# Optimization experiments

Hardware: AMD Instinct MI355X
Metric: run time of the kernel (lower is better)

Reference implementation:

```python
import jax, jax.numpy as jnp
import numpy as np

B, D, H, K = 32768, 64, 512, 8
P = 3 * K - 1            # widths(K) + heights(K) + interior derivatives(K-1)
BOUND = 4.0
MIN_BIN = 1e-3           # min bin width/height fraction
MIN_DERIV = 1e-3


def setup_inputs() -> dict:
    key = jax.random.key(0)
    k0, k1, k2, k3 = jax.random.split(key, 4)
    x = jax.random.normal(k0, (B, D), jnp.float32) * 2.0
    W1 = jax.random.normal(k1, (H, D), jnp.float32) / np.sqrt(D)
    b1 = jnp.zeros((H,), jnp.float32)
    W2 = jax.random.normal(k2, (D * P, H), jnp.float32) / np.sqrt(H)
    b2 = jax.random.normal(k3, (D * P,), jnp.float32) * 0.01
    m_in = np.arange(1, D + 1)                      # input degrees 1..D
    m_hid = (np.arange(H) % (D - 1)) + 1            # hidden degrees 1..D-1
    M1 = jnp.asarray((m_hid[:, None] >= m_in[None, :]).astype(np.float32))   # [H, D]
    m_out = (np.arange(D * P) // P) + 1             # output degree = dim index + 1
    M2 = jnp.asarray((m_out[:, None] > m_hid[None, :]).astype(np.float32))   # [D*P, H]
    return {"x": x, "W1": W1, "b1": b1, "W2": W2, "b2": b2, "M1": M1, "M2": M2}


def _rqs(x, w_un, h_un, d_un):
    """Monotonic rational-quadratic spline (elementwise over [B, D]).
    w_un, h_un: [B, D, K] unnormalized widths/heights; d_un: [B, D, K-1].
    Returns (y [B, D], logabsdet [B, D])."""
    f32 = x.dtype
    w = jax.nn.softmax(w_un, axis=-1)
    hh = jax.nn.softmax(h_un, axis=-1)
    w = MIN_BIN + (1.0 - MIN_BIN * K) * w
    hh = MIN_BIN + (1.0 - MIN_BIN * K) * hh
    edge_lo = jnp.full(w.shape[:-1] + (1,), -BOUND, f32)
    edge_hi = jnp.full(w.shape[:-1] + (1,), BOUND, f32)
    # knot positions [B, D, K+1] with exact endpoints at +-BOUND
    xk = jnp.concatenate([edge_lo, -BOUND + 2.0 * BOUND * jnp.cumsum(w, -1)[..., :-1], edge_hi], -1)
    yk = jnp.concatenate([edge_lo, -BOUND + 2.0 * BOUND * jnp.cumsum(hh, -1)[..., :-1], edge_hi], -1)
    widths = xk[..., 1:] - xk[..., :-1]
    heights = yk[..., 1:] - yk[..., :-1]
    ones = jnp.ones(w.shape[:-1] + (1,), f32)
    # boundary derivatives fixed to 1 (identity outside the box)
    d = jnp.concatenate([ones, MIN_DERIV + jax.nn.softplus(d_un), ones], -1)  # [B, D, K+1]

    inside = (x >= -BOUND) & (x <= BOUND)
    xc = jnp.clip(x, -BOUND, BOUND)
    # bucketize: index of containing bin
    idx = jnp.clip(jnp.sum((xc[..., None] >= xk).astype(jnp.int32), -1) - 1, 0, K - 1)

    def g(a, off=0):
        return jnp.take_along_axis(a, idx[..., None] + off, axis=-1)[..., 0]

    x_k, y_k = g(xk), g(yk)
    w_k, h_k = g(widths), g(heights)
    d_k, d_k1 = g(d), g(d, 1)
    s = h_k / w_k
    theta = (xc - x_k) / w_k
    t1m = theta * (1.0 - theta)
    num = h_k * (s * theta * theta + d_k * t1m)
    den = s + (d_k1 + d_k - 2.0 * s) * t1m
    y_in = y_k + num / den
    dnum = s * s * (d_k1 * theta * theta + 2.0 * s * t1m + d_k * (1.0 - theta) ** 2)
    ld_in = jnp.log(dnum) - 2.0 * jnp.log(den)
    y = jnp.where(inside, y_in, x)
    ld = jnp.where(inside, ld_in, 0.0)
    return y, ld


def _forward(x, W1, b1, W2, b2, M1, M2):
    hmid = jax.nn.relu(x @ (W1 * M1).T + b1)          # [B, H]
    params = (hmid @ (W2 * M2).T + b2).reshape(x.shape[0], D, P)
    w_un = params[..., :K]
    h_un = params[..., K:2 * K]
    d_un = params[..., 2 * K:]
    z, ld = _rqs(x, w_un, h_un, d_un)
    return z, jnp.sum(ld, axis=-1)                    # logDet per example


def reference(x, W1, b1, W2, b2, M1, M2):
    return _forward(x, W1, b1, W2, b2, M1, M2)
```

## Files before the change

### kernel.cpp

```cpp
#include <hip/hip_runtime.h>
#include <math.h>

#define NB    32768
#define DDIM  64
#define HDIM  512
#define PDIM  23
#define KBINS 8
#define BM    32
#define NCOLS (DDIM * PDIM)
#define CHUNK 368
#define PSTRIDE 372
#define NTILES 92

#define RQ_BOUND  4.0f
#define RQ_MINBIN 0.001f
#define RQ_MINDER 0.001f

typedef __attribute__((ext_vector_type(8))) _Float16 half8;
typedef __attribute__((ext_vector_type(4))) float f32x4;
typedef unsigned short ushort_t;

__global__ __launch_bounds__(256) void prep_frag(const float* __restrict__ W1,
                                                 const float* __restrict__ W2,
                                                 _Float16* __restrict__ W1g,
                                                 _Float16* __restrict__ W2g) {
    const int gid = blockIdx.x * 256 + threadIdx.x;
    const int NW1 = 32 * 2 * 64;
    if (gid < NW1) {
        const int lane = gid & 63;
        const int tk   = gid >> 6;
        const int kt   = tk & 1, ht = tk >> 1;
        const int h = ht * 16 + (lane & 15);
        const int k = kt * 32 + (lane >> 4) * 8;
        const float* src = W1 + h * DDIM + k;
        const int hm63 = h % 63;
        half8 v;
        #pragma unroll
        for (int e = 0; e < 8; ++e)
            v[e] = (_Float16)(((k + e) <= hm63) ? src[e] : 0.0f);
        *(half8*)(W1g + (size_t)gid * 8) = v;
    } else {
        const int g2 = gid - NW1;
        if (g2 < NTILES * 16 * 64) {
            const int lane = g2 & 63;
            const int tk   = g2 >> 6;
            const int kt   = tk & 15, T = tk >> 4;
            const int col  = T * 16 + (lane & 15);
            const int k    = kt * 32 + (lane >> 4) * 8;
            const float* src = W2 + (size_t)col * HDIM + k;
            const int d = col / PDIM;
            half8 v;
            #pragma unroll
            for (int e = 0; e < 8; ++e)
                v[e] = (_Float16)((d > ((k + e) % 63)) ? src[e] : 0.0f);
            *(half8*)(W2g + (size_t)g2 * 8) = v;
        }
    }
}

__device__ __forceinline__ float fexp(float v)  { return __expf(v); }
__device__ __forceinline__ float flog(float v)  { return __logf(v); }
__device__ __forceinline__ float fdiv(float a, float b) { return __fdividef(a, b); }

__device__ __forceinline__ void rqs_eval(const float* prm, float xorig,
                                         float& yo, float& ldo) {
    const float xc = fminf(fmaxf(xorig, -RQ_BOUND), RQ_BOUND);
    const bool inside = (xorig >= -RQ_BOUND) && (xorig <= RQ_BOUND);
    const float CNORM = 1.0f - RQ_MINBIN * KBINS;

    float xk[KBINS + 1], yk[KBINS + 1], dd[KBINS + 1];
    {
        float e[KBINS]; float s = 0.0f;
        #pragma unroll
        for (int i = 0; i < KBINS; ++i) { e[i] = fexp(prm[i]); s += e[i]; }
        const float cinv = CNORM * fdiv(1.0f, s);
        float c = 0.0f;
        xk[0] = -RQ_BOUND;
        #pragma unroll
        for (int i = 0; i < KBINS; ++i) {
            c += fmaf(e[i], cinv, RQ_MINBIN);
            xk[i + 1] = fmaf(c, 2.0f * RQ_BOUND, -RQ_BOUND);
        }
        xk[KBINS] = RQ_BOUND;
    }
    {
        float e[KBINS]; float s = 0.0f;
        #pragma unroll
        for (int i = 0; i < KBINS; ++i) { e[i] = fexp(prm[8 + i]); s += e[i]; }
        const float cinv = CNORM * fdiv(1.0f, s);
        float c = 0.0f;
        yk[0] = -RQ_BOUND;
        #pragma unroll
        for (int i = 0; i < KBINS; ++i) {
            c += fmaf(e[i], cinv, RQ_MINBIN);
            yk[i + 1] = fmaf(c, 2.0f * RQ_BOUND, -RQ_BOUND);
        }
        yk[KBINS] = RQ_BOUND;
    }
    dd[0] = 1.0f;
    #pragma unroll
    for (int i = 0; i < KBINS - 1; ++i)
        dd[i + 1] = RQ_MINDER + flog(1.0f + fexp(prm[16 + i]));
    dd[KBINS] = 1.0f;

    int idx = 0;
    #pragma unroll
    for (int i = 1; i < KBINS; ++i) idx += (xc >= xk[i]) ? 1 : 0;

    float x_k = xk[0], x_k1 = xk[1];
    float y_k = yk[0], y_k1 = yk[1];
    float d_k = dd[0], d_k1 = dd[1];
    #pragma unroll
    for (int i = 1; i < KBINS; ++i) {
        const bool mm = (idx == i);
        x_k  = mm ? xk[i]     : x_k;
        x_k1 = mm ? xk[i + 1] : x_k1;
        y_k  = mm ? yk[i]     : y_k;
        y_k1 = mm ? yk[i + 1] : y_k1;
        d_k  = mm ? dd[i]     : d_k;
        d_k1 = mm ? dd[i + 1] : d_k1;
    }

    const float w_k = x_k1 - x_k;
    const float h_k = y_k1 - y_k;
    const float rw  = fdiv(1.0f, w_k);
    const float s   = h_k * rw;
    const float th  = (xc - x_k) * rw;
    const float omt = 1.0f - th;
    const float t1m = th * omt;
    const float num = h_k * (s * th * th + d_k * t1m);
    const float den = s + (d_k1 + d_k - 2.0f * s) * t1m;
    const float yin = y_k + fdiv(num, den);
    const float dnum = s * s * (d_k1 * th * th + 2.0f * s * t1m + d_k * omt * omt);
    const float ldin = flog(fdiv(dnum, den * den));

    yo  = inside ? yin : xorig;
    ldo = inside ? ldin : 0.0f;
}

__global__ __launch_bounds__(512, 4) void fused_flow(
    const float* __restrict__ x,  const float* __restrict__ b1,
    const float* __restrict__ b2, const _Float16* __restrict__ W1g,
    const _Float16* __restrict__ W2g,
    float* __restrict__ z_out, float* __restrict__ ld_out)
{
    __shared__ __align__(16) ushort_t hm[BM * 512];
    __shared__ __align__(16) float pstage[BM * PSTRIDE];

    const int t    = threadIdx.x;
    const int row0 = blockIdx.x * BM;
    const int wv   = t >> 6;
    const int lane = t & 63;
    const int l15  = lane & 15;
    const int lg   = lane >> 4;

    char* hmB = (char*)hm;

    {
        f32x4 acc1[4][2];
        #pragma unroll
        for (int j = 0; j < 4; ++j)
            #pragma unroll
            for (int m = 0; m < 2; ++m) acc1[j][m] = (f32x4){0.f, 0.f, 0.f, 0.f};

        #pragma unroll
        for (int kt = 0; kt < 2; ++kt) {
            half8 a[2];
            #pragma unroll
            for (int m = 0; m < 2; ++m) {
                const float* xr = x + (size_t)(row0 + m * 16 + l15) * DDIM + kt * 32 + lg * 8;
                const float4 xa = *(const float4*)(xr);
                const float4 xb = *(const float4*)(xr + 4);
                a[m][0] = (_Float16)xa.x; a[m][1] = (_Float16)xa.y;
                a[m][2] = (_Float16)xa.z; a[m][3] = (_Float16)xa.w;
                a[m][4] = (_Float16)xb.x; a[m][5] = (_Float16)xb.y;
                a[m][6] = (_Float16)xb.z; a[m][7] = (_Float16)xb.w;
            }
            #pragma unroll
            for (int j = 0; j < 4; ++j) {
                const half8 b = *(const half8*)(W1g + (size_t)(wv * 4 + j) * 1024 + kt * 512 + lane * 8);
                #pragma unroll
                for (int m = 0; m < 2; ++m)
                    acc1[j][m] = __builtin_amdgcn_mfma_f32_16x16x32_f16(a[m], b, acc1[j][m], 0, 0, 0);
            }
        }
        #pragma unroll
        for (int j = 0; j < 4; ++j) {
            const int h = (wv * 4 + j) * 16 + l15;
            const float bias = b1[h];
            #pragma unroll
            for (int m = 0; m < 2; ++m) {
                #pragma unroll
                for (int q = 0; q < 4; ++q) {
                    const int r = m * 16 + lg * 4 + q;
                    const _Float16 hv = (_Float16)fmaxf(acc1[j][m][q] + bias, 0.0f);
                    *(ushort_t*)(hmB + r * 1024 + ((h * 2) ^ ((r & 7) << 4))) =
                        __builtin_bit_cast(ushort_t, hv);
                }
            }
        }
    }
    __syncthreads();

    float ldacc = 0.0f;
    const int srow = t >> 4;
    const int sd   = t & 15;
    const int tbase = wv * 3;

    const _Float16* w2base[3];
    #pragma unroll
    for (int i = 0; i < 3; ++i) {
        const int tile = (tbase + i < 23) ? (tbase + i) : 22;
        w2base[i] = W2g + (size_t)tile * 8192 + lane * 8;
    }

    half8 pfb0[3], pfb1[3];
    #pragma unroll
    for (int i = 0; i < 3; ++i) {
        pfb0[i] = *(const half8*)(w2base[i]);
        pfb1[i] = *(const half8*)(w2base[i] + 512);
    }

    for (int c = 0; c < 4; ++c) {
        f32x4 acc[3][2];
        #pragma unroll
        for (int i = 0; i < 3; ++i)
            #pragma unroll
            for (int m = 0; m < 2; ++m) acc[i][m] = (f32x4){0.f, 0.f, 0.f, 0.f};

        const size_t coff = (size_t)c * (23 * 8192);

        #pragma unroll
        for (int kt = 0; kt < 2; ++kt) {
            half8 ah[2];
            #pragma unroll
            for (int m = 0; m < 2; ++m) {
                const int r  = m * 16 + l15;
                const int kb = (kt * 32 + lg * 8) * 2;
                ah[m] = *(const half8*)(hmB + r * 1024 + (kb ^ ((r & 7) << 4)));
            }
            #pragma unroll
            for (int i = 0; i < 3; ++i) {
                const half8 bf = (kt == 0) ? pfb0[i] : pfb1[i];
                #pragma unroll
                for (int m = 0; m < 2; ++m)
                    acc[i][m] = __builtin_amdgcn_mfma_f32_16x16x32_f16(ah[m], bf, acc[i][m], 0, 0, 0);
            }
        }

        #pragma unroll 2
        for (int kt = 2; kt < 16; ++kt) {
            half8 ah[2];
            #pragma unroll
            for (int m = 0; m < 2; ++m) {
                const int r  = m * 16 + l15;
                const int kb = (kt * 32 + lg * 8) * 2;
                ah[m] = *(const half8*)(hmB + r * 1024 + (kb ^ ((r & 7) << 4)));
            }
            half8 bfr[3];
            #pragma unroll
            for (int i = 0; i < 3; ++i)
                bfr[i] = *(const half8*)(w2base[i] + coff + kt * 512);
            #pragma unroll
            for (int i = 0; i < 3; ++i)
                #pragma unroll
                for (int m = 0; m < 2; ++m)
                    acc[i][m] = __builtin_amdgcn_mfma_f32_16x16x32_f16(ah[m], bfr[i], acc[i][m], 0, 0, 0);
        }

        __syncthreads();

        #pragma unroll
        for (int i = 0; i < 3; ++i) {
            if (tbase + i < 23) {
                const int lcol = (tbase + i) * 16 + l15;
                #pragma unroll
                for (int m = 0; m < 2; ++m)
                    #pragma unroll
                    for (int q = 0; q < 4; ++q)
                        pstage[(m * 16 + lg * 4 + q) * PSTRIDE + lcol] = acc[i][m][q];
            }
        }
        __syncthreads();

        {
            const size_t ncoff = (size_t)(c < 3 ? c + 1 : 3) * (23 * 8192);
            #pragma unroll
            for (int i = 0; i < 3; ++i) {
                pfb0[i] = *(const half8*)(w2base[i] + ncoff);
                pfb1[i] = *(const half8*)(w2base[i] + ncoff + 512);
            }
        }

        {
            const int d = c * 16 + sd;
            float prm[PDIM];
            #pragma unroll
            for (int p = 0; p < PDIM; ++p)
                prm[p] = pstage[srow * PSTRIDE + sd * PDIM + p] + b2[d * PDIM + p];
            const float xv = x[(size_t)(row0 + srow) * DDIM + d];
            float yv, lv;
            rqs_eval(prm, xv, yv, lv);
            z_out[(size_t)(row0 + srow) * DDIM + d] = yv;
            ldacc += lv;
        }
    }

    ldacc += __shfl_xor(ldacc, 1, 64);
    ldacc += __shfl_xor(ldacc, 2, 64);
    ldacc += __shfl_xor(ldacc, 4, 64);
    ldacc += __shfl_xor(ldacc, 8, 64);
    if (sd == 0) ld_out[row0 + srow] = ldacc;
}

extern "C" void kernel_launch(void* const* d_in, const int* in_sizes, int n_in,
                              void* d_out, int out_size, void* d_ws, size_t ws_size,
                              hipStream_t stream) {
    (void)in_sizes; (void)n_in; (void)out_size; (void)ws_size;
    const float* x  = (const float*)d_in[0];
    const float* W1 = (const float*)d_in[1];
    const float* b1 = (const float*)d_in[2];
    const float* W2 = (const float*)d_in[3];
    const float* b2 = (const float*)d_in[4];

    _Float16* W1g = (_Float16*)d_ws;
    _Float16* W2g = W1g + HDIM * DDIM;
    float* z  = (float*)d_out;
    float* ld = z + (size_t)NB * DDIM;

    const int n_groups = 32 * 2 * 64 + NTILES * 16 * 64;
    prep_frag<<<(n_groups + 255) / 256, 256, 0, stream>>>(W1, W2, W1g, W2g);
    fused_flow<<<NB / BM, 512, 0, stream>>>(x, b1, b2, W1g, W2g, z, ld);
}
```

Baseline: 92.47 us.

## Give each wave a private column strip to remove per-chunk block barriers

Each wave now owns a 46-column strip per chunk, covering two full output dims, made of three overlapping 16-column MFMA tiles. The weight fragments are repacked in prep so each wave's tiles are contiguous. The wave stages its results in its own shared-memory region and evaluates the spline for its own dims, so the two __syncthreads per chunk and the cross-wave register prefetch go away. Outputs are gathered through shared memory and written as coalesced float4 stores. In exchange it does some redundant MFMA work on the overlapping columns, uses more shared memory, and drops the explicit prefetch of the next chunk's weights.

```diff
diff --git a/kernel.cpp b/kernel.cpp
--- a/kernel.cpp
+++ b/kernel.cpp
@@ -8,9 +8,9 @@
 #define KBINS 8
 #define BM    32
 #define NCOLS (DDIM * PDIM)
-#define CHUNK 368
-#define PSTRIDE 372
-#define NTILES 92
+#define CHUNKC 368
+#define STRIPW 46
+#define PSTR  47
 
 #define RQ_BOUND  4.0f
 #define RQ_MINBIN 0.001f
@@ -41,11 +41,15 @@
         *(half8*)(W1g + (size_t)gid * 8) = v;
     } else {
         const int g2 = gid - NW1;
-        if (g2 < NTILES * 16 * 64) {
+        if (g2 < 96 * 16 * 64) {
             const int lane = g2 & 63;
             const int tk   = g2 >> 6;
-            const int kt   = tk & 15, T = tk >> 4;
-            const int col  = T * 16 + (lane & 15);
+            const int kt   = tk & 15, tt = tk >> 4;
+            const int c    = tt / 24;
+            const int r    = tt % 24;
+            const int wvs  = r / 3, i = r % 3;
+            const int colbase = c * CHUNKC + wvs * STRIPW + (i < 2 ? 16 * i : 30);
+            const int col  = colbase + (lane & 15);
             const int k    = kt * 32 + (lane >> 4) * 8;
             const float* src = W2 + (size_t)col * HDIM + k;
             const int d = col / PDIM;
@@ -145,7 +149,7 @@
     float* __restrict__ z_out, float* __restrict__ ld_out)
 {
     __shared__ __align__(16) ushort_t hm[BM * 512];
-    __shared__ __align__(16) float pstage[BM * PSTRIDE];
+    __shared__ __align__(16) float pstage[8 * BM * PSTR];
 
     const int t    = threadIdx.x;
     const int row0 = blockIdx.x * BM;
@@ -154,7 +158,8 @@
     const int l15  = lane & 15;
     const int lg   = lane >> 4;
 
-    char* hmB = (char*)hm;
+    char*  hmB = (char*)hm;
+    float* pw  = pstage + wv * (BM * PSTR);
 
     {
         f32x4 acc1[4][2];
@@ -202,54 +207,27 @@
     }
     __syncthreads();
 
+    const int srow  = lane & 31;
+    const int hi    = lane >> 5;
+    const int dbase = 2 * wv + hi;
+
+    const float* xrow = x + (size_t)(row0 + srow) * DDIM + dbase;
+    const float xs0 = xrow[0], xs1 = xrow[16], xs2 = xrow[32], xs3 = xrow[48];
+
     float ldacc = 0.0f;
-    const int srow = t >> 4;
-    const int sd   = t & 15;
-    const int tbase = wv * 3;
-
-    const _Float16* w2base[3];
-    #pragma unroll
-    for (int i = 0; i < 3; ++i) {
-        const int tile = (tbase + i < 23) ? (tbase + i) : 22;
-        w2base[i] = W2g + (size_t)tile * 8192 + lane * 8;
-    }
-
-    half8 pfb0[3], pfb1[3];
-    #pragma unroll
-    for (int i = 0; i < 3; ++i) {
-        pfb0[i] = *(const half8*)(w2base[i]);
-        pfb1[i] = *(const half8*)(w2base[i] + 512);
-    }
-
-    for (int c = 0; c < 4; ++c) {
+    float z0, z1, z2, z3;
+
+    auto CSTEP = [&](int C, float xv, float& zv) {
         f32x4 acc[3][2];
         #pragma unroll
         for (int i = 0; i < 3; ++i)
             #pragma unroll
             for (int m = 0; m < 2; ++m) acc[i][m] = (f32x4){0.f, 0.f, 0.f, 0.f};
 
-        const size_t coff = (size_t)c * (23 * 8192);
-
-        #pragma unroll
-        for (int kt = 0; kt < 2; ++kt) {
-            half8 ah[2];
-            #pragma unroll
-            for (int m = 0; m < 2; ++m) {
-                const int r  = m * 16 + l15;
-                const int kb = (kt * 32 + lg * 8) * 2;
-                ah[m] = *(const half8*)(hmB + r * 1024 + (kb ^ ((r & 7) << 4)));
-            }
-            #pragma unroll
-            for (int i = 0; i < 3; ++i) {
-                const half8 bf = (kt == 0) ? pfb0[i] : pfb1[i];
-                #pragma unroll
-                for (int m = 0; m < 2; ++m)
-                    acc[i][m] = __builtin_amdgcn_mfma_f32_16x16x32_f16(ah[m], bf, acc[i][m], 0, 0, 0);
-            }
-        }
-
-        #pragma unroll 2
-        for (int kt = 2; kt < 16; ++kt) {
+        const _Float16* sbase = W2g + ((size_t)(C * 24 + wv * 3)) * 8192 + lane * 8;
+
+        #pragma unroll 4
+        for (int kt = 0; kt < 16; ++kt) {
             half8 ah[2];
             #pragma unroll
             for (int m = 0; m < 2; ++m) {
@@ -260,7 +238,7 @@
             half8 bfr[3];
             #pragma unroll
             for (int i = 0; i < 3; ++i)
-                bfr[i] = *(const half8*)(w2base[i] + coff + kt * 512);
+                bfr[i] = *(const half8*)(sbase + (size_t)i * 8192 + kt * 512);
             #pragma unroll
             for (int i = 0; i < 3; ++i)
                 #pragma unroll
@@ -268,49 +246,60 @@
                     acc[i][m] = __builtin_amdgcn_mfma_f32_16x16x32_f16(ah[m], bfr[i], acc[i][m], 0, 0, 0);
         }
 
-        __syncthreads();
-
         #pragma unroll
         for (int i = 0; i < 3; ++i) {
-            if (tbase + i < 23) {
-                const int lcol = (tbase + i) * 16 + l15;
+            const int lcol = (i < 2 ? 16 * i : 30) + l15;
+            #pragma unroll
+            for (int m = 0; m < 2; ++m)
                 #pragma unroll
-                for (int m = 0; m < 2; ++m)
-                    #pragma unroll
-                    for (int q = 0; q < 4; ++q)
-                        pstage[(m * 16 + lg * 4 + q) * PSTRIDE + lcol] = acc[i][m][q];
-            }
-        }
-        __syncthreads();
+                for (int q = 0; q < 4; ++q)
+                    pw[(m * 16 + lg * 4 + q) * PSTR + lcol] = acc[i][m][q];
+        }
 
         {
-            const size_t ncoff = (size_t)(c < 3 ? c + 1 : 3) * (23 * 8192);
-            #pragma unroll
-            for (int i = 0; i < 3; ++i) {
-                pfb0[i] = *(const half8*)(w2base[i] + ncoff);
-                pfb1[i] = *(const half8*)(w2base[i] + ncoff + 512);
-            }
-        }
-
-        {
-            const int d = c * 16 + sd;
+            const float* bp = b2 + (size_t)(C * 16 + dbase) * PDIM;
             float prm[PDIM];
             #pragma unroll
             for (int p = 0; p < PDIM; ++p)
-                prm[p] = pstage[srow * PSTRIDE + sd * PDIM + p] + b2[d * PDIM + p];
-            const float xv = x[(size_t)(row0 + srow) * DDIM + d];
+                prm[p] = pw[srow * PSTR + hi * PDIM + p] + bp[p];
             float yv, lv;
             rqs_eval(prm, xv, yv, lv);
-            z_out[(size_t)(row0 + srow) * DDIM + d] = yv;
+            zv = yv;
             ldacc += lv;
         }
-    }
-
-    ldacc += __shfl_xor(ldacc, 1, 64);
-    ldacc += __shfl_xor(ldacc, 2, 64);
-    ldacc += __shfl_xor(ldacc, 4, 64);
-    ldacc += __shfl_xor(ldacc, 8, 64);
-    if (sd == 0) ld_out[row0 + srow] = ldacc;
+    };
+
+    CSTEP(0, xs0, z0);
+    CSTEP(1, xs1, z1);
+    CSTEP(2, xs2, z2);
+    CSTEP(3, xs3, z3);
+
+    ldacc += __shfl_xor(ldacc, 32, 64);
+    __syncthreads();
+
+    pstage[srow * 65 +      dbase] = z0;
+    pstage[srow * 65 + 16 + dbase] = z1;
+    pstage[srow * 65 + 32 + dbase] = z2;
+    pstage[srow * 65 + 48 + dbase] = z3;
+    if (lane < 32) pstage[2080 + srow * 8 + wv] = ldacc;
+    __syncthreads();
+
+    {
+        const int r  = t >> 4;
+        const int d0 = (t & 15) * 4;
+        float4 zv;
+        zv.x = pstage[r * 65 + d0 + 0];
+        zv.y = pstage[r * 65 + d0 + 1];
+        zv.z = pstage[r * 65 + d0 + 2];
+        zv.w = pstage[r * 65 + d0 + 3];
+        *(float4*)(z_out + (size_t)(row0 + r) * DDIM + d0) = zv;
+    }
+    if (t < BM) {
+        float s = 0.0f;
+        #pragma unroll
+        for (int w = 0; w < 8; ++w) s += pstage[2080 + t * 8 + w];
+        ld_out[row0 + t] = s;
+    }
 }
 
 extern "C" void kernel_launch(void* const* d_in, const int* in_sizes, int n_in,
@@ -328,7 +317,7 @@
     float* z  = (float*)d_out;
     float* ld = z + (size_t)NB * DDIM;
 
-    const int n_groups = 32 * 2 * 64 + NTILES * 16 * 64;
+    const int n_groups = 32 * 2 * 64 + 96 * 16 * 64;
     prep_frag<<<(n_groups + 255) / 256, 256, 0, stream>>>(W1, W2, W1g, W2g);
     fused_flow<<<NB / BM, 512, 0, stream>>>(x, b1, b2, W1g, W2g, z, ld);
 }
```

Measured after the change: 140.4 us. 51.9% more time.
